# Optimization experiments

Measured on AMD Instinct MI355X. Metric: run time of the kernel, lower is better.

Reference implementation:

```python
import jax, jax.numpy as jnp
import numpy as np

B, S, D = 2, 2048, 1024
H = 16
DH = D // H
FFN = 4096
EPS = 1e-5
SCALE = 1.0 / np.sqrt(DH).astype(np.float32)


def layer_norm(x, g, b):
    mu = jnp.mean(x, axis=-1, keepdims=True)
    var = jnp.mean(jnp.square(x - mu), axis=-1, keepdims=True)
    return (x - mu) * jax.lax.rsqrt(var + EPS) * g + b


def setup_inputs() -> dict:
    key = jax.random.key(0)
    ks = jax.random.split(key, 12)
    std = 0.02
    return {
        "x": jax.random.normal(ks[0], (B, S, D), dtype=jnp.float32),
        "mask": jax.random.randint(ks[1], (B, S), 0, 2, dtype=jnp.int32),
        "w_qkv": jax.random.normal(ks[2], (D, 3 * D), dtype=jnp.float32) * std,
        "w_out": jax.random.normal(ks[3], (D, D), dtype=jnp.float32) * std,
        "b_out": jnp.zeros((D,), dtype=jnp.float32),
        "g1": jnp.ones((D,), dtype=jnp.float32),
        "be1": jnp.zeros((D,), dtype=jnp.float32),
        "g2": jnp.ones((D,), dtype=jnp.float32),
        "be2": jnp.zeros((D,), dtype=jnp.float32),
        "w1": jax.random.normal(ks[4], (D, FFN), dtype=jnp.float32) * std,
        "b1": jnp.zeros((FFN,), dtype=jnp.float32),
        "w2": jax.random.normal(ks[5], (FFN, D), dtype=jnp.float32) * std,
        "b2": jnp.zeros((D,), dtype=jnp.float32),
    }


def reference(x, mask, w_qkv, w_out, b_out, g1, be1, g2, be2, w1, b1, w2, b2):
    # --- pre-norm self-attention ---
    h = layer_norm(x, g1, be1)                              # [B,S,D]
    qkv = (h @ w_qkv).reshape(B, S, 3, H, DH)               # [B,S,3,H,Dh]
    q, k, v = [jnp.transpose(qkv[:, :, i], (0, 2, 1, 3)) for i in range(3)]  # [B,H,S,Dh]
    scores = jnp.einsum("bhqd,bhkd->bhqk", q, k) * SCALE    # [B,H,S,S]
    key_mask = (mask != 0)[:, None, None, :]                # [B,1,1,S]
    scores = jnp.where(key_mask, scores, -1e9)
    attn = jax.nn.softmax(scores, axis=-1)
    out = jnp.einsum("bhqk,bhkd->bhqd", attn, v)            # [B,H,S,Dh]
    out = jnp.transpose(out, (0, 2, 1, 3)).reshape(B, S, D)
    x = x + (out @ w_out + b_out)
    # --- pre-norm FFN ---
    h2 = layer_norm(x, g2, be2)
    ffn = jax.nn.relu(h2 @ w1 + b1) @ w2 + b2
    return x + ffn
```

## Files before the change

kernel.cpp:

```cpp
#include <hip/hip_runtime.h>

typedef unsigned short u16;
typedef __bf16 bf16x8 __attribute__((ext_vector_type(8)));
typedef float f32x4 __attribute__((ext_vector_type(4)));

typedef __attribute__((address_space(1))) const void* as1cv;
typedef __attribute__((address_space(3))) void* as3v;

__device__ __forceinline__ u16 f2bf(float f) {
  union { float f; unsigned u; } v;
  v.f = f;
  unsigned r = (v.u + 0x7fffu + ((v.u >> 16) & 1u)) >> 16;
  return (u16)r;
}

__device__ __forceinline__ unsigned cvtpk(float lo, float hi) {
  unsigned r;
  asm("v_cvt_pk_bf16_f32 %0, %1, %2" : "=v"(r) : "v"(lo), "v"(hi));
  return r;
}

__device__ __forceinline__ void gload16(const void* g, void* l) {
  __builtin_amdgcn_global_load_lds((as1cv)g, (as3v)l, 16, 0, 0);
}

__global__ __launch_bounds__(256)
void ln_kernel(const float* __restrict__ x, const float* __restrict__ g,
               const float* __restrict__ be, u16* __restrict__ out) {
  __shared__ float red[8];
  const int row = blockIdx.x;
  const int tid = threadIdx.x;
  const float4 v = ((const float4*)(x + (size_t)row * 1024))[tid];
  float s = v.x + v.y + v.z + v.w;
#pragma unroll
  for (int off = 1; off < 64; off <<= 1) s += __shfl_xor(s, off, 64);
  const int wv = tid >> 6, lane = tid & 63;
  if (lane == 0) red[wv] = s;
  __syncthreads();
  s = red[0] + red[1] + red[2] + red[3];
  const float mu = s * (1.0f / 1024.0f);
  const float d0 = v.x - mu, d1 = v.y - mu, d2 = v.z - mu, d3 = v.w - mu;
  float q = d0 * d0 + d1 * d1 + d2 * d2 + d3 * d3;
#pragma unroll
  for (int off = 1; off < 64; off <<= 1) q += __shfl_xor(q, off, 64);
  if (lane == 0) red[4 + wv] = q;
  __syncthreads();
  q = red[4] + red[5] + red[6] + red[7];
  const float inv = rsqrtf(q * (1.0f / 1024.0f) + 1e-5f);
  const float4 gv = ((const float4*)g)[tid];
  const float4 bv = ((const float4*)be)[tid];
  unsigned p0 = (unsigned)f2bf(d0 * inv * gv.x + bv.x) |
                ((unsigned)f2bf(d1 * inv * gv.y + bv.y) << 16);
  unsigned p1 = (unsigned)f2bf(d2 * inv * gv.z + bv.z) |
                ((unsigned)f2bf(d3 * inv * gv.w + bv.w) << 16);
  uint2 o; o.x = p0; o.y = p1;
  *(uint2*)(out + (size_t)row * 1024 + tid * 4) = o;
}

__global__ __launch_bounds__(256)
void transpose_all(const float* __restrict__ i0, u16* __restrict__ o0,
                   const float* __restrict__ i1, u16* __restrict__ o1,
                   const float* __restrict__ i2, u16* __restrict__ o2,
                   const float* __restrict__ i3, u16* __restrict__ o3) {
  __shared__ float t[32][33];
  int id = blockIdx.x;
  const float* in; u16* out; int K, N, nx;
  if (id < 3072)      { in = i0; out = o0; K = 1024; N = 3072; nx = 96; }
  else if (id < 4096) { id -= 3072; in = i1; out = o1; K = 1024; N = 1024; nx = 32; }
  else if (id < 8192) { id -= 4096; in = i2; out = o2; K = 1024; N = 4096; nx = 128; }
  else                { id -= 8192; in = i3; out = o3; K = 4096; N = 1024; nx = 32; }
  const int n0 = (id % nx) * 32, k0 = (id / nx) * 32;
  const int tx = threadIdx.x & 31, ty = threadIdx.x >> 5;
  for (int r = ty; r < 32; r += 8)
    t[r][tx] = in[(size_t)(k0 + r) * N + n0 + tx];
  __syncthreads();
  for (int r = ty; r < 32; r += 8)
    out[(size_t)(n0 + r) * K + k0 + tx] = f2bf(t[tx][r]);
}

template<int BIAS, int RELU, int RES, int MODE, int NSPLIT>
__global__ __launch_bounds__(256, 2)
void gemm_bt(const u16* __restrict__ A, const u16* __restrict__ Bt,
             const float* __restrict__ bias, const float* __restrict__ res,
             void* __restrict__ C, u16* __restrict__ vt,
             int M, int N, int K, int kChunk) {
  __shared__ u16 As[2][4096];
  __shared__ u16 Bs[2][4096];
  const int tid = threadIdx.x;
  const int wv = tid >> 6, lane = tid & 63;
  const int z = (NSPLIT > 1) ? (int)(blockIdx.x % NSPLIT) : 0;
  const int bm = (int)(blockIdx.x / NSPLIT) * 128;
  const int bn = blockIdx.y * 128;
  const int wr = wv >> 1, wc = wv & 1;
  const int l16 = lane & 15, lk = (lane >> 4) * 8;
  const int srow = lane >> 2, sc = (lane & 3) * 8;

  f32x4 acc[4][4] = {};

  const int kb = z * kChunk;
  const u16* Ag = A + (size_t)(bm + wv * 32 + srow) * K + kb + sc;
  const u16* Bg = Bt + (size_t)(bn + wv * 32 + srow) * K + kb + sc;

#define STAGE_BT(buf, ko)                                          \
  do {                                                             \
    gload16(Ag + (ko), &As[buf][wv * 1024]);                       \
    gload16(Ag + (size_t)16 * K + (ko), &As[buf][wv * 1024 + 512]);\
    gload16(Bg + (ko), &Bs[buf][wv * 1024]);                       \
    gload16(Bg + (size_t)16 * K + (ko), &Bs[buf][wv * 1024 + 512]);\
  } while (0)

  const int nst = kChunk >> 5;
  STAGE_BT(0, 0);
  if (nst > 1) STAGE_BT(1, 32);

  for (int t = 0; t < nst; ++t) {
    const int cur = t & 1;
    if (t + 1 < nst) asm volatile("s_waitcnt vmcnt(4)" ::: "memory");
    else             asm volatile("s_waitcnt vmcnt(0)" ::: "memory");
    __builtin_amdgcn_s_barrier();
    asm volatile("" ::: "memory");
    bf16x8 af[4], bfv[4];
#pragma unroll
    for (int i = 0; i < 4; i++)
      af[i] = *(const bf16x8*)&As[cur][(wr * 64 + i * 16 + l16) * 32 + lk];
#pragma unroll
    for (int j = 0; j < 4; j++)
      bfv[j] = *(const bf16x8*)&Bs[cur][(wc * 64 + j * 16 + l16) * 32 + lk];
    __builtin_amdgcn_s_setprio(1);
#pragma unroll
    for (int i = 0; i < 4; i++)
#pragma unroll
      for (int j = 0; j < 4; j++)
        acc[i][j] = __builtin_amdgcn_mfma_f32_16x16x32_bf16(af[i], bfv[j], acc[i][j], 0, 0, 0);
    __builtin_amdgcn_s_setprio(0);
    asm volatile("" ::: "memory");
    __builtin_amdgcn_s_barrier();
    asm volatile("" ::: "memory");
    if (t + 2 < nst) STAGE_BT(cur, (t + 2) * 32);
  }
#undef STAGE_BT

#pragma unroll
  for (int i = 0; i < 4; i++) {
#pragma unroll
    for (int j = 0; j < 4; j++) {
      const int col = bn + wc * 64 + j * 16 + l16;
      const float bv = (BIAS && z == 0) ? bias[col] : 0.0f;
      if (MODE == 3 && bn >= 2048) {
        const int cc = col - 2048, h = cc >> 6, d = cc & 63;
        const int row0 = bm + wr * 64 + i * 16 + (lane >> 4) * 4;
        const int bb = row0 >> 11, kv0 = row0 & 2047;
        const int p0 = (kv0 & 32) | (((kv0 >> 2) & 3) << 3) | (((kv0 >> 4) & 1) << 2);
        uint2 o;
        o.x = (unsigned)f2bf(acc[i][j][0]) | ((unsigned)f2bf(acc[i][j][1]) << 16);
        o.y = (unsigned)f2bf(acc[i][j][2]) | ((unsigned)f2bf(acc[i][j][3]) << 16);
        *(uint2*)(vt + ((size_t)(bb * 16 + h) * 64 + d) * 2048 + (kv0 & ~63) + p0) = o;
      } else {
#pragma unroll
        for (int r = 0; r < 4; r++) {
          const int row = bm + wr * 64 + i * 16 + (lane >> 4) * 4 + r;
          float v = acc[i][j][r] + bv;
          if (RELU) v = fmaxf(v, 0.0f);
          if (RES) v += res[(size_t)row * N + col];
          if (MODE == 2)       atomicAdd((float*)C + (size_t)row * N + col, v);
          else if (MODE == 0)  ((float*)C)[(size_t)row * N + col] = v;
          else                 ((u16*)C)[(size_t)row * N + col] = f2bf(v);
        }
      }
    }
  }
}

__global__ __launch_bounds__(256, 4)
void attn3(const u16* __restrict__ qkv, const u16* __restrict__ vT,
           const int* __restrict__ mask, u16* __restrict__ aout) {
  __shared__ u16 KsS[2][4096];
  __shared__ u16 VsS[2][4096];
  __shared__ float mbL[2048];

  const int tid = threadIdx.x;
  const int wv = tid >> 6, lane = tid & 63;
  const int l16 = lane & 15, lh = lane >> 4;
  const int bh = blockIdx.x, b = bh >> 4, h = bh & 15;
  const int q0 = blockIdx.y * 64 + wv * 16;

  {
    const int4* srcm = (const int4*)(mask + b * 2048);
    float4* dstm = (float4*)mbL;
#pragma unroll
    for (int u = 0; u < 2; ++u) {
      const int4 mv = srcm[tid + u * 256];
      float4 f;
      f.x = mv.x ? 0.f : -1.4426950408889634e9f;
      f.y = mv.y ? 0.f : -1.4426950408889634e9f;
      f.z = mv.z ? 0.f : -1.4426950408889634e9f;
      f.w = mv.w ? 0.f : -1.4426950408889634e9f;
      dstm[tid + u * 256] = f;
    }
  }

  bf16x8 qf[2];
#pragma unroll
  for (int c = 0; c < 2; ++c)
    qf[c] = *(const bf16x8*)(qkv + (size_t)(b * 2048 + q0 + l16) * 3072 + h * 64 + c * 32 + 8 * lh);

  const int rs = (l16 & 7) << 4;
  const int koff0 = ((16 * lh) ^ rs) >> 1;
  const int koff1 = ((64 + 16 * lh) ^ rs) >> 1;
  const int voff0 = koff0, voff1 = koff1;

  const int rl0 = wv * 8 + (lane >> 3);
  const int rl1 = 32 + wv * 8 + (lane >> 3);
  const int glog = (lane & 7) ^ ((lane >> 3) & 7);
  const u16* kg0 = qkv + (size_t)(b * 2048 + rl0) * 3072 + 1024 + h * 64 + 8 * glog;
  const u16* kg1 = qkv + (size_t)(b * 2048 + rl1) * 3072 + 1024 + h * 64 + 8 * glog;
  const u16* vg0 = vT + ((size_t)bh * 64 + rl0) * 2048 + 8 * glog;
  const u16* vg1 = vT + ((size_t)bh * 64 + rl1) * 2048 + 8 * glog;

  gload16(kg0, &KsS[0][wv * 512]);
  gload16(kg1, &KsS[0][2048 + wv * 512]);
  gload16(vg0, &VsS[0][wv * 512]);
  gload16(vg1, &VsS[0][2048 + wv * 512]);
  kg0 += 64 * 3072; kg1 += 64 * 3072; vg0 += 64; vg1 += 64;

  const float CL2 = 0.125f * 1.4426950408889634f;
  float lacc = 0.f;
  f32x4 oT[4] = {};

  for (int t = 0; t < 32; ++t) {
    asm volatile("s_waitcnt vmcnt(0)" ::: "memory");
    __syncthreads();
    const int cur = t & 1;
    if (t + 1 < 32) {
      const int nx = cur ^ 1;
      gload16(kg0, &KsS[nx][wv * 512]);
      gload16(kg1, &KsS[nx][2048 + wv * 512]);
      gload16(vg0, &VsS[nx][wv * 512]);
      gload16(vg1, &VsS[nx][2048 + wv * 512]);
      kg0 += 64 * 3072; kg1 += 64 * 3072; vg0 += 64; vg1 += 64;
    }

    const u16* Kb = &KsS[cur][0];
    const u16* Vb = &VsS[cur][0];

    f32x4 mbc[4];
#pragma unroll
    for (int n = 0; n < 4; ++n)
      mbc[n] = *(const f32x4*)&mbL[t * 64 + n * 16 + 4 * lh];

    f32x4 s[4] = {};
    __builtin_amdgcn_s_setprio(1);
#pragma unroll
    for (int c = 0; c < 2; ++c) {
      const int ko = c ? koff1 : koff0;
      bf16x8 kf[4];
#pragma unroll
      for (int n = 0; n < 4; ++n)
        kf[n] = *(const bf16x8*)(Kb + (n * 16 + l16) * 64 + ko);
#pragma unroll
      for (int n = 0; n < 4; ++n)
        s[n] = __builtin_amdgcn_mfma_f32_16x16x32_bf16(kf[n], qf[c], s[n], 0, 0, 0);
    }
    __builtin_amdgcn_s_setprio(0);

#pragma unroll
    for (int n = 0; n < 4; ++n)
#pragma unroll
      for (int j = 0; j < 4; ++j) {
        const float p = __builtin_exp2f(fmaf(s[n][j], CL2, mbc[n][j]));
        s[n][j] = p;
        lacc += p;
      }

    union U8 { unsigned u[4]; bf16x8 v; };
    U8 pa[2];
#pragma unroll
    for (int u = 0; u < 2; ++u) {
      pa[u].u[0] = cvtpk(s[2 * u][0], s[2 * u][1]);
      pa[u].u[1] = cvtpk(s[2 * u][2], s[2 * u][3]);
      pa[u].u[2] = cvtpk(s[2 * u + 1][0], s[2 * u + 1][1]);
      pa[u].u[3] = cvtpk(s[2 * u + 1][2], s[2 * u + 1][3]);
    }

    __builtin_amdgcn_s_setprio(1);
#pragma unroll
    for (int u = 0; u < 2; ++u) {
      const int vo = u ? voff1 : voff0;
#pragma unroll
      for (int D = 0; D < 4; ++D) {
        const bf16x8 va = *(const bf16x8*)(Vb + (D * 16 + l16) * 64 + vo);
        oT[D] = __builtin_amdgcn_mfma_f32_16x16x32_bf16(va, pa[u].v, oT[D], 0, 0, 0);
      }
    }
    __builtin_amdgcn_s_setprio(0);
  }

  lacc += __shfl_xor(lacc, 16, 64);
  lacc += __shfl_xor(lacc, 32, 64);
  const float rr = 1.0f / lacc;
#pragma unroll
  for (int D = 0; D < 4; ++D) {
    uint2 o;
    o.x = cvtpk(oT[D][0] * rr, oT[D][1] * rr);
    o.y = cvtpk(oT[D][2] * rr, oT[D][3] * rr);
    *(uint2*)(aout + (size_t)(b * 2048 + q0 + l16) * 1024 + h * 64 + D * 16 + 4 * lh) = o;
  }
}

extern "C" void kernel_launch(void* const* d_in, const int* in_sizes, int n_in,
                              void* d_out, int out_size, void* d_ws, size_t ws_size,
                              hipStream_t stream) {
  (void)in_sizes; (void)n_in; (void)out_size; (void)ws_size;
  const float* x     = (const float*)d_in[0];
  const int*   mask  = (const int*)d_in[1];
  const float* w_qkv = (const float*)d_in[2];
  const float* w_out = (const float*)d_in[3];
  const float* b_out = (const float*)d_in[4];
  const float* g1    = (const float*)d_in[5];
  const float* be1   = (const float*)d_in[6];
  const float* g2    = (const float*)d_in[7];
  const float* be2   = (const float*)d_in[8];
  const float* w1    = (const float*)d_in[9];
  const float* b1    = (const float*)d_in[10];
  const float* w2    = (const float*)d_in[11];
  const float* b2    = (const float*)d_in[12];
  float* out = (float*)d_out;

  char* ws = (char*)d_ws;
  u16* hA    = (u16*)(ws);
  u16* wqkvT = (u16*)(ws + 8388608);
  u16* woutT = (u16*)(ws + 14680064);
  u16* w1T   = (u16*)(ws + 16777216);
  u16* w2T   = (u16*)(ws + 25165824);
  u16* qkv   = (u16*)(ws + 33554432);
  u16* ffn1  = (u16*)(ws + 33554432);
  u16* vTb   = (u16*)(ws + 67108864);
  u16* aout  = (u16*)(ws + 75497472);

  ln_kernel<<<4096, 256, 0, stream>>>(x, g1, be1, hA);
  transpose_all<<<12288, 256, 0, stream>>>(w_qkv, wqkvT, w_out, woutT, w1, w1T, w2, w2T);
  gemm_bt<0, 0, 0, 3, 1><<<dim3(32, 24), 256, 0, stream>>>(hA, wqkvT, nullptr, nullptr, qkv, vTb, 4096, 3072, 1024, 1024);
  attn3<<<dim3(32, 32), 256, 0, stream>>>(qkv, vTb, mask, aout);
  gemm_bt<1, 0, 1, 0, 1><<<dim3(32, 8), 256, 0, stream>>>(aout, woutT, b_out, x, out, nullptr, 4096, 1024, 1024, 1024);
  ln_kernel<<<4096, 256, 0, stream>>>(out, g2, be2, hA);
  gemm_bt<1, 1, 0, 1, 1><<<dim3(32, 32), 256, 0, stream>>>(hA, w1T, b1, nullptr, ffn1, nullptr, 4096, 4096, 1024, 1024);
  gemm_bt<1, 0, 0, 2, 2><<<dim3(64, 8), 256, 0, stream>>>(ffn1, w2T, b2, nullptr, out, nullptr, 4096, 1024, 4096, 2048);
}
```

Before: 266.6 us.

## Triple-buffer GEMM LDS stages with XOR swizzle and split MFMA phases

Moves the bf16 GEMM main loop from double to triple buffering in LDS. With the extra buffer, the second barrier per K-step can be dropped and the next-next tile loads issue mid-iteration, interleaved with two halves of the MFMA work. The LDS layout also gets an XOR swizzle on the k-chunk index to cut bank conflicts on the fragment reads. LDS use rises to 48KB per block, which may limit occupancy under launch_bounds(256,2).

After: 267.5 us. About the same (+0.3%).

```diff
diff --git a/kernel.cpp b/kernel.cpp
--- a/kernel.cpp
+++ b/kernel.cpp
@@ -84,61 +84,73 @@
              const float* __restrict__ bias, const float* __restrict__ res,
              void* __restrict__ C, u16* __restrict__ vt,
              int M, int N, int K, int kChunk) {
-  __shared__ u16 As[2][4096];
-  __shared__ u16 Bs[2][4096];
+  __shared__ u16 As[3][4096];
+  __shared__ u16 Bs[3][4096];
   const int tid = threadIdx.x;
   const int wv = tid >> 6, lane = tid & 63;
   const int z = (NSPLIT > 1) ? (int)(blockIdx.x % NSPLIT) : 0;
   const int bm = (int)(blockIdx.x / NSPLIT) * 128;
   const int bn = blockIdx.y * 128;
   const int wr = wv >> 1, wc = wv & 1;
-  const int l16 = lane & 15, lk = (lane >> 4) * 8;
-  const int srow = lane >> 2, sc = (lane & 3) * 8;
+  const int l16 = lane & 15, lh = lane >> 4;
+
+  const int ssk = ((lane & 3) ^ ((lane >> 2) & 3)) << 3;
+  const int rdk = (lh ^ (l16 & 3)) << 3;
 
   f32x4 acc[4][4] = {};
 
   const int kb = z * kChunk;
-  const u16* Ag = A + (size_t)(bm + wv * 32 + srow) * K + kb + sc;
-  const u16* Bg = Bt + (size_t)(bn + wv * 32 + srow) * K + kb + sc;
-
-#define STAGE_BT(buf, ko)                                          \
-  do {                                                             \
-    gload16(Ag + (ko), &As[buf][wv * 1024]);                       \
-    gload16(Ag + (size_t)16 * K + (ko), &As[buf][wv * 1024 + 512]);\
-    gload16(Bg + (ko), &Bs[buf][wv * 1024]);                       \
-    gload16(Bg + (size_t)16 * K + (ko), &Bs[buf][wv * 1024 + 512]);\
-  } while (0)
+  const u16* Ag = A + (size_t)(bm + wv * 16 + (lane >> 2)) * K + kb + ssk;
+  const u16* Bg = Bt + (size_t)(bn + wv * 16 + (lane >> 2)) * K + kb + ssk;
+
+#define STG_A(buf, ko)  do { \
+    gload16(Ag + (ko), &As[buf][wv * 512]); \
+    gload16(Ag + (size_t)64 * K + (ko), &As[buf][2048 + wv * 512]); } while (0)
+#define STG_B(buf, ko)  do { \
+    gload16(Bg + (ko), &Bs[buf][wv * 512]); \
+    gload16(Bg + (size_t)64 * K + (ko), &Bs[buf][2048 + wv * 512]); } while (0)
 
   const int nst = kChunk >> 5;
-  STAGE_BT(0, 0);
-  if (nst > 1) STAGE_BT(1, 32);
-
+  STG_A(0, 0); STG_B(0, 0);
+  if (nst > 1) { STG_A(1, 32); STG_B(1, 32); }
+
+  int cur = 0;
   for (int t = 0; t < nst; ++t) {
-    const int cur = t & 1;
     if (t + 1 < nst) asm volatile("s_waitcnt vmcnt(4)" ::: "memory");
     else             asm volatile("s_waitcnt vmcnt(0)" ::: "memory");
     __builtin_amdgcn_s_barrier();
     asm volatile("" ::: "memory");
+    const int nxb = (cur + 2 >= 3) ? cur - 1 : cur + 2;
     bf16x8 af[4], bfv[4];
 #pragma unroll
     for (int i = 0; i < 4; i++)
-      af[i] = *(const bf16x8*)&As[cur][(wr * 64 + i * 16 + l16) * 32 + lk];
-#pragma unroll
-    for (int j = 0; j < 4; j++)
-      bfv[j] = *(const bf16x8*)&Bs[cur][(wc * 64 + j * 16 + l16) * 32 + lk];
+      af[i] = *(const bf16x8*)&As[cur][(wr * 64 + i * 16 + l16) * 32 + rdk];
+#pragma unroll
+    for (int j = 0; j < 2; j++)
+      bfv[j] = *(const bf16x8*)&Bs[cur][(wc * 64 + j * 16 + l16) * 32 + rdk];
+    if (t + 2 < nst) STG_A(nxb, (t + 2) * 32);
     __builtin_amdgcn_s_setprio(1);
 #pragma unroll
     for (int i = 0; i < 4; i++)
 #pragma unroll
-      for (int j = 0; j < 4; j++)
+      for (int j = 0; j < 2; j++)
         acc[i][j] = __builtin_amdgcn_mfma_f32_16x16x32_bf16(af[i], bfv[j], acc[i][j], 0, 0, 0);
     __builtin_amdgcn_s_setprio(0);
-    asm volatile("" ::: "memory");
-    __builtin_amdgcn_s_barrier();
-    asm volatile("" ::: "memory");
-    if (t + 2 < nst) STAGE_BT(cur, (t + 2) * 32);
-  }
-#undef STAGE_BT
+#pragma unroll
+    for (int j = 2; j < 4; j++)
+      bfv[j] = *(const bf16x8*)&Bs[cur][(wc * 64 + j * 16 + l16) * 32 + rdk];
+    if (t + 2 < nst) STG_B(nxb, (t + 2) * 32);
+    __builtin_amdgcn_s_setprio(1);
+#pragma unroll
+    for (int i = 0; i < 4; i++)
+#pragma unroll
+      for (int j = 2; j < 4; j++)
+        acc[i][j] = __builtin_amdgcn_mfma_f32_16x16x32_bf16(af[i], bfv[j], acc[i][j], 0, 0, 0);
+    __builtin_amdgcn_s_setprio(0);
+    cur = (cur + 1 == 3) ? 0 : cur + 1;
+  }
+#undef STG_A
+#undef STG_B
 
 #pragma unroll
   for (int i = 0; i < 4; i++) {
```
